# Performance work log

Hardware: AMD Instinct MI355X
Metric: run time of the kernel (lower is better)

## Reference

```python
import jax, jax.numpy as jnp
import numpy as np
import math

B, S, D = 2, 2048, 1024
H, HKV, HD = 16, 4, 64
SF = 4
SD = HD // SF  # sparsity proj dim = 16
TEMP = 1.0
INIT_STD = 0.02


def rope(qk):
    # qk: [b, h, s, d]
    d = qk.shape[-1]
    theta = 1.0 / (10000.0 ** (jnp.arange(0, d, 2, dtype=jnp.float32) / d))  # [d/2]
    s = jnp.arange(qk.shape[2], dtype=jnp.float32)
    freqs = jnp.outer(s, theta)                     # [s, d/2]
    freqs = jnp.concatenate([freqs, freqs], -1)     # [s, d]
    qk1, qk2 = jnp.split(qk, 2, axis=-1)
    rot = jnp.concatenate([-qk2, qk1], -1)
    return qk * jnp.cos(freqs) + rot * jnp.sin(freqs)


def setup_inputs() -> dict:
    key = jax.random.key(0)
    ks = jax.random.split(key, 8)
    x = jax.random.normal(ks[0], (B, S, D), dtype=jnp.float32)
    Wq = jax.random.normal(ks[1], (D, D), dtype=jnp.float32) * INIT_STD
    Wk = jax.random.normal(ks[2], (HKV * HD, D), dtype=jnp.float32) * INIT_STD
    Wv = jax.random.normal(ks[3], (HKV * HD, D), dtype=jnp.float32) * INIT_STD
    Wo = jax.random.normal(ks[4], (D, D), dtype=jnp.float32) * INIT_STD
    bo = jnp.zeros((D,), dtype=jnp.float32)
    Ws = jax.random.normal(ks[5], (SD, HD), dtype=jnp.float32) * INIT_STD
    bs = jnp.zeros((SD,), dtype=jnp.float32)
    return {"x": x, "Wq": Wq, "Wk": Wk, "Wv": Wv, "Wo": Wo, "bo": bo, "Ws": Ws, "bs": bs}


def reference(x, Wq, Wk, Wv, Wo, bo, Ws, bs):
    b, s, _ = x.shape
    # projections (torch Linear: x @ W.T)
    q = (x @ Wq.T).reshape(b, s, H, HD).transpose(0, 2, 1, 3)     # [b,H,s,hd]
    k = (x @ Wk.T).reshape(b, s, HKV, HD).transpose(0, 2, 1, 3)   # [b,Hkv,s,hd]
    v = (x @ Wv.T).reshape(b, s, HKV, HD).transpose(0, 2, 1, 3)
    q = rope(q)
    k = rope(k)
    n_rep = H // HKV
    k = jnp.repeat(k, n_rep, axis=1)  # [b,H,s,hd]
    v = jnp.repeat(v, n_rep, axis=1)
    # low-rank sparsity gate
    q_sp = q @ Ws.T + bs              # [b,H,s,sd]
    k_sp = k @ Ws.T + bs
    sp_scores = jnp.einsum('bhid,bhjd->bhij', q_sp, k_sp) / math.sqrt(SD)
    gate = jax.nn.sigmoid(sp_scores / TEMP)
    attn = jnp.einsum('bhid,bhjd->bhij', q, k) / math.sqrt(HD)
    attn = attn * gate
    causal = jnp.triu(jnp.ones((s, s), dtype=bool), k=1)
    attn = jnp.where(causal, -jnp.inf, attn)
    w = jax.nn.softmax(attn, axis=-1)
    out = jnp.einsum('bhij,bhjd->bhid', w, v)               # [b,H,s,hd]
    out = out.transpose(0, 2, 1, 3).reshape(b, s, H * HD)   # [b,s,D]
    return out @ Wo.T + bo
```

## Files before the change

### kernel.cpp

```cpp
#include <hip/hip_runtime.h>
#include <math.h>

#define B_ 2
#define S_ 2048
#define D_ 1024
#define H_ 16
#define HKV_ 4
#define HD_ 64
#define SD_ 16

typedef __attribute__((ext_vector_type(8))) short bf16x8;
typedef __attribute__((ext_vector_type(4))) float f32x4;
typedef __attribute__((ext_vector_type(8))) unsigned short us8;
typedef __attribute__((ext_vector_type(4))) unsigned short us4;

#define LOG2E 1.4426950408889634f

__device__ __forceinline__ unsigned short f2bf(float f) {
  unsigned int u = __builtin_bit_cast(unsigned int, f);
  u += 0x7fffu + ((u >> 16) & 1u);
  return (unsigned short)(u >> 16);
}

__device__ __forceinline__ void gload16(const unsigned short* g, unsigned short* l) {
  __builtin_amdgcn_global_load_lds(
      (const __attribute__((address_space(1))) unsigned int*)g,
      (__attribute__((address_space(3))) unsigned int*)l, 16, 0, 0);
}

__global__ __launch_bounds__(256) void convert_bf16(
    const float* __restrict__ x, const float* __restrict__ wq,
    const float* __restrict__ wk, const float* __restrict__ wv,
    const float* __restrict__ wo, unsigned short* __restrict__ xb,
    unsigned short* __restrict__ wqkv, unsigned short* __restrict__ wob) {
  const int blk = blockIdx.x;
  const float* src;
  unsigned short* dst;
  int off;
  if (blk < 2048)      { src = x;  dst = xb;             off = blk * 2048; }
  else if (blk < 2560) { src = wq; dst = wqkv;           off = (blk - 2048) * 2048; }
  else if (blk < 2688) { src = wk; dst = wqkv + 1048576; off = (blk - 2560) * 2048; }
  else if (blk < 2816) { src = wv; dst = wqkv + 1310720; off = (blk - 2688) * 2048; }
  else                 { src = wo; dst = wob;            off = (blk - 2816) * 2048; }
  const int i = off + threadIdx.x * 8;
  float4 a = *(const float4*)(src + i);
  float4 b = *(const float4*)(src + i + 4);
  us8 o;
  o[0] = f2bf(a.x); o[1] = f2bf(a.y); o[2] = f2bf(a.z); o[3] = f2bf(a.w);
  o[4] = f2bf(b.x); o[5] = f2bf(b.y); o[6] = f2bf(b.z); o[7] = f2bf(b.w);
  *(us8*)(dst + i) = o;
}

__global__ __launch_bounds__(256) void gemm_bf16(
    const unsigned short* __restrict__ A, const unsigned short* __restrict__ Bm,
    const float* __restrict__ bias, float* __restrict__ C, int N) {
  __shared__ unsigned short As[64 * 64];
  __shared__ unsigned short Bs[128 * 64];
  const int tid = threadIdx.x;
  const int w = tid >> 6, lane = tid & 63;
  const int nm = lane & 15, quad = lane >> 4;
  const int m0 = blockIdx.y * 64, n0 = blockIdx.x * 128;
  const int wn = w * 32;

  f32x4 acc[4][2] = {};
  int arow[2], acol[2], brow[4], bcol[4];
#pragma unroll
  for (int it = 0; it < 2; ++it) {
    int s = it * 256 + tid;
    arow[it] = s >> 3;
    acol[it] = ((s & 7) ^ (arow[it] & 7)) * 8;
  }
#pragma unroll
  for (int it = 0; it < 4; ++it) {
    int s = it * 256 + tid;
    brow[it] = s >> 3;
    bcol[it] = ((s & 7) ^ (brow[it] & 7)) * 8;
  }

  for (int k0 = 0; k0 < 1024; k0 += 64) {
    __syncthreads();
#pragma unroll
    for (int it = 0; it < 2; ++it)
      gload16(A + (size_t)(m0 + arow[it]) * 1024 + k0 + acol[it],
              &As[(it * 256 + w * 64) * 8]);
#pragma unroll
    for (int it = 0; it < 4; ++it)
      gload16(Bm + (size_t)(n0 + brow[it]) * 1024 + k0 + bcol[it],
              &Bs[(it * 256 + w * 64) * 8]);
    __syncthreads();

#pragma unroll
    for (int ks = 0; ks < 2; ++ks) {
      const int cq = ks * 4 + quad;
      bf16x8 af[4], bfr[2];
#pragma unroll
      for (int mi = 0; mi < 4; ++mi) {
        const int m = mi * 16 + nm;
        af[mi] = *(const bf16x8*)&As[(m * 8 + (cq ^ (m & 7))) * 8];
      }
#pragma unroll
      for (int ni = 0; ni < 2; ++ni) {
        const int n = wn + ni * 16 + nm;
        bfr[ni] = *(const bf16x8*)&Bs[(n * 8 + (cq ^ (n & 7))) * 8];
      }
#pragma unroll
      for (int mi = 0; mi < 4; ++mi)
#pragma unroll
        for (int ni = 0; ni < 2; ++ni)
          acc[mi][ni] = __builtin_amdgcn_mfma_f32_16x16x32_bf16(
              af[mi], bfr[ni], acc[mi][ni], 0, 0, 0);
    }
  }

  float bv[2] = {0.f, 0.f};
  if (bias) {
#pragma unroll
    for (int ni = 0; ni < 2; ++ni) bv[ni] = bias[n0 + wn + ni * 16 + nm];
  }
#pragma unroll
  for (int mi = 0; mi < 4; ++mi) {
#pragma unroll
    for (int r = 0; r < 4; ++r) {
      const int row = m0 + mi * 16 + quad * 4 + r;
      float* crow = C + (size_t)row * N + n0 + wn + nm;
#pragma unroll
      for (int ni = 0; ni < 2; ++ni) crow[ni * 16] = acc[mi][ni][r] + bv[ni];
    }
  }
}

__global__ __launch_bounds__(256) void gemm_bf16_128(
    const unsigned short* __restrict__ A, const unsigned short* __restrict__ Bm,
    const float* __restrict__ bias, float* __restrict__ C, int N) {
  __shared__ unsigned short As[128 * 64];
  __shared__ unsigned short Bs[128 * 64];
  const int tid = threadIdx.x;
  const int w = tid >> 6, lane = tid & 63;
  const int nm = lane & 15, quad = lane >> 4;
  const int m0 = blockIdx.y * 128, n0 = blockIdx.x * 128;
  const int wm = (w >> 1) * 64, wn = (w & 1) * 64;

  f32x4 acc[4][4] = {};
  int srow[4], scol[4];
#pragma unroll
  for (int it = 0; it < 4; ++it) {
    int s = it * 256 + tid;
    srow[it] = s >> 3;
    scol[it] = ((s & 7) ^ (srow[it] & 7)) * 8;
  }

  for (int k0 = 0; k0 < 1024; k0 += 64) {
    __syncthreads();
#pragma unroll
    for (int it = 0; it < 4; ++it) {
      gload16(A + (size_t)(m0 + srow[it]) * 1024 + k0 + scol[it],
              &As[(it * 256 + w * 64) * 8]);
      gload16(Bm + (size_t)(n0 + srow[it]) * 1024 + k0 + scol[it],
              &Bs[(it * 256 + w * 64) * 8]);
    }
    __syncthreads();

#pragma unroll
    for (int ks = 0; ks < 2; ++ks) {
      const int cq = ks * 4 + quad;
      bf16x8 af[4], bfr[4];
#pragma unroll
      for (int mi = 0; mi < 4; ++mi) {
        const int m = wm + mi * 16 + nm;
        af[mi] = *(const bf16x8*)&As[(m * 8 + (cq ^ (m & 7))) * 8];
      }
#pragma unroll
      for (int ni = 0; ni < 4; ++ni) {
        const int n = wn + ni * 16 + nm;
        bfr[ni] = *(const bf16x8*)&Bs[(n * 8 + (cq ^ (n & 7))) * 8];
      }
#pragma unroll
      for (int mi = 0; mi < 4; ++mi)
#pragma unroll
        for (int ni = 0; ni < 4; ++ni)
          acc[mi][ni] = __builtin_amdgcn_mfma_f32_16x16x32_bf16(
              af[mi], bfr[ni], acc[mi][ni], 0, 0, 0);
    }
  }

  float bv[4] = {0.f, 0.f, 0.f, 0.f};
  if (bias) {
#pragma unroll
    for (int ni = 0; ni < 4; ++ni) bv[ni] = bias[n0 + wn + ni * 16 + nm];
  }
#pragma unroll
  for (int mi = 0; mi < 4; ++mi) {
#pragma unroll
    for (int r = 0; r < 4; ++r) {
      const int row = m0 + wm + mi * 16 + quad * 4 + r;
      float* crow = C + (size_t)row * N + n0 + wn + nm;
#pragma unroll
      for (int ni = 0; ni < 4; ++ni) crow[ni * 16] = acc[mi][ni][r] + bv[ni];
    }
  }
}

__global__ __launch_bounds__(256) void rope_scatter(
    const float* __restrict__ P, const float* __restrict__ Ws,
    const float* __restrict__ bs, unsigned short* __restrict__ qh,
    unsigned short* __restrict__ kh, unsigned short* __restrict__ qsp,
    unsigned short* __restrict__ ksp) {
  __shared__ float wsl[16 * 64];
  __shared__ float bsl[16];
  __shared__ float rbuf[4][64];
  const int tid = threadIdx.x;
  const int row = blockIdx.x;
  const int b = row >> 11;
  const int s = row & 2047;
  {
    *(float4*)&wsl[tid * 4] = *(const float4*)&Ws[tid * 4];
    if (tid < 16) bsl[tid] = bs[tid];
  }
  __syncthreads();
  const int w = tid >> 6, lane = tid & 63;
  const int i = lane & 31, halfu = lane >> 5;
  const float theta = powf(10000.f, -((float)(2 * i) * (1.f / 64.f)));
  const float f = (float)s * theta;
  const float cf = cosf(f);
  const float sf = sinf(f);
  for (int slot = w; slot < 20; slot += 4) {
    float val = P[(size_t)row * 1536 + slot * 64 + lane];
    float partner = __shfl_xor(val, 32);
    float rot = halfu ? partner : -partner;
    float r = val * cf + rot * sf;
    unsigned short* dst;
    unsigned short* spdst;
    float qscale, spscale;
    if (slot < 16) {
      dst = qh + ((size_t)(b * 16 + slot) * 2048 + s) * 64;
      spdst = qsp + ((size_t)(b * 16 + slot) * 2048 + s) * 16;
      qscale = 0.125f * LOG2E; spscale = 0.25f * LOG2E;
    } else {
      int hh = slot - 16;
      dst = kh + ((size_t)(b * 4 + hh) * 2048 + s) * 64;
      spdst = ksp + ((size_t)(b * 4 + hh) * 2048 + s) * 16;
      qscale = 1.f; spscale = 1.f;
    }
    dst[lane] = f2bf(r * qscale);
    rbuf[w][lane] = r;
    int p = lane >> 4, j = lane & 15;
    float partial = 0.f;
#pragma unroll
    for (int t = 0; t < 16; ++t)
      partial += wsl[j * 64 + p * 16 + t] * rbuf[w][p * 16 + t];
    partial += __shfl_xor(partial, 16);
    partial += __shfl_xor(partial, 32);
    if (p == 0) spdst[j] = f2bf((partial + bsl[j]) * spscale);
  }
}

__global__ __launch_bounds__(256) void v_transpose(
    const float* __restrict__ proj, unsigned short* __restrict__ vt) {
  __shared__ unsigned short t_[64 * 72];
  const int bkv = blockIdx.y;
  const int s0 = blockIdx.x * 64;
  const int b = bkv >> 2, hkv = bkv & 3;
  const int tid = threadIdx.x;
  const int sl = tid >> 2;
  const int c0 = (tid & 3) * 16;
  const float* src = proj + ((size_t)b * 2048 + s0 + sl) * 1536 + 1280 + hkv * 64 + c0;
  us8 o0, o1;
#pragma unroll
  for (int t = 0; t < 8; ++t) { o0[t] = f2bf(src[t]); o1[t] = f2bf(src[8 + t]); }
  *(us8*)&t_[sl * 72 + c0] = o0;
  *(us8*)&t_[sl * 72 + c0 + 8] = o1;
  __syncthreads();
  const int d = tid >> 2;
  const int sc_ = (tid & 3) * 16;
  us8 w0, w1;
#pragma unroll
  for (int t = 0; t < 8; ++t) w0[t] = t_[(sc_ + t) * 72 + d];
#pragma unroll
  for (int t = 0; t < 8; ++t) w1[t] = t_[(sc_ + 8 + t) * 72 + d];
  unsigned short* dst = vt + (size_t)bkv * 131072 + (size_t)d * 2048 + s0 + sc_;
  *(us8*)dst = w0;
  *(us8*)(dst + 8) = w1;
}

template <bool MASK>
__device__ __forceinline__ void attn_tile(
    const unsigned short* __restrict__ Ksb, const unsigned short* __restrict__ Vsb,
    const unsigned short* __restrict__ Kspb_, unsigned short* __restrict__ pw,
    bf16x8 qa0, bf16x8 qa1, bf16x8 qspa, int j0, int qrow0, int nm, int quad,
    int ws, float l_r[4], f32x4 O[4]) {
#pragma unroll
  for (int stl = 0; stl < 2; ++stl) {
    const int st = ws * 2 + stl;
    if (MASK && (j0 + st * 16 > qrow0 + 15)) {
#pragma unroll
      for (int r = 0; r < 4; ++r) {
        const int prow = quad * 4 + r;
        const int chunk = (stl * 2 + (nm >> 3)) ^ ((prow ^ (prow >> 2)) & 3);
        pw[(prow * 4 + chunk) * 8 + (nm & 7)] = 0;
      }
      continue;
    }
    const int krow = st * 16 + nm;
    const int r7 = krow & 7;
    bf16x8 kb0 = *(const bf16x8*)&Ksb[(krow * 8 + (quad ^ r7)) * 8];
    bf16x8 kb1 = *(const bf16x8*)&Ksb[(krow * 8 + ((4 + quad) ^ r7)) * 8];
    bf16x8 gb = *(const bf16x8*)&Kspb_[(krow * 2 + (quad & 1)) * 8];
    f32x4 z = {0.f, 0.f, 0.f, 0.f};
    f32x4 s = __builtin_amdgcn_mfma_f32_16x16x32_bf16(qa0, kb0, z, 0, 0, 0);
    s = __builtin_amdgcn_mfma_f32_16x16x32_bf16(qa1, kb1, s, 0, 0, 0);
    f32x4 g = __builtin_amdgcn_mfma_f32_16x16x32_bf16(qspa, gb, z, 0, 0, 0);
#pragma unroll
    for (int r = 0; r < 4; ++r) {
      float gate = __builtin_amdgcn_rcpf(1.f + __builtin_amdgcn_exp2f(-g[r]));
      float v = s[r] * gate;
      if (MASK) {
        const bool edge = (j0 + st * 16 + 15 > qrow0);
        if (edge) {
          const int col = j0 + st * 16 + nm;
          const int rowg = qrow0 + quad * 4 + r;
          v = (col > rowg) ? -INFINITY : v;
        }
      }
      float p = __builtin_amdgcn_exp2f(v);
      l_r[r] += p;
      const int prow = quad * 4 + r;
      const int chunk = (stl * 2 + (nm >> 3)) ^ ((prow ^ (prow >> 2)) & 3);
      pw[(prow * 4 + chunk) * 8 + (nm & 7)] = f2bf(p);
    }
  }

  bf16x8 pa = *(const bf16x8*)&pw[(nm * 4 + (quad ^ ((nm ^ (nm >> 2)) & 3))) * 8];
#pragma unroll
  for (int dt = 0; dt < 4; ++dt) {
    const int vrow = dt * 16 + nm;
    bf16x8 vb = *(const bf16x8*)&Vsb[(vrow * 8 + ((ws * 4 + quad) ^ (vrow & 7))) * 8];
    O[dt] = __builtin_amdgcn_mfma_f32_16x16x32_bf16(pa, vb, O[dt], 0, 0, 0);
  }
}

__global__ __launch_bounds__(512) void attn_kernel(
    const unsigned short* __restrict__ qh, const unsigned short* __restrict__ kh,
    const unsigned short* __restrict__ vt, const unsigned short* __restrict__ qsp,
    const unsigned short* __restrict__ ksp, unsigned short* __restrict__ ao) {
  __shared__ unsigned short Ks[2][64 * 64];
  __shared__ unsigned short Vs[2][64 * 64];
  __shared__ unsigned short Ksp[2][64 * 16];
  __shared__ unsigned short Pw[8][16 * 32];
  __shared__ float Ox[4][16][64];
  __shared__ float Lx[4][4][64];

  const int tid = threadIdx.x;
  const int w = tid >> 6;
  const int ws = w >> 2;
  const int wr = w & 3;
  const int lane = tid & 63;
  const int nm = lane & 15;
  const int quad = lane >> 4;
  const int bh = blockIdx.y;
  const int b = bh >> 4, h = bh & 15;
  const int hkv = h >> 2;
  const size_t kbase = (size_t)(b * 4 + hkv) * 2048 * 64;
  const size_t vbase = (size_t)(b * 4 + hkv) * 131072;
  const size_t kspb = (size_t)(b * 4 + hkv) * 2048 * 16;

  const int Lc = tid;
  const int sr = Lc >> 3;
  const int sc = ((Lc & 7) ^ (sr & 7)) * 8;
  unsigned short* pw = &Pw[w][0];

#define STAGE(BUF, J0)                                                         \
  {                                                                            \
    gload16(kh + kbase + (size_t)((J0) + sr) * 64 + sc,                        \
            &Ks[BUF][(w * 64) * 8]);                                           \
    gload16(vt + vbase + (size_t)sr * 2048 + (J0) + sc,                        \
            &Vs[BUF][(w * 64) * 8]);                                           \
    if (w < 2) {                                                               \
      gload16(ksp + kspb + (size_t)((J0) + (Lc >> 1)) * 16 + (Lc & 1) * 8,     \
              &Ksp[BUF][w * 512]);                                             \
    }                                                                          \
  }

  const int qxA = 31 - blockIdx.x;
  const int qxB = blockIdx.x;
  const int qrow0A = qxA * 64 + wr * 16;
  const int qrow0B = qxB * 64 + wr * 16;

  const size_t qbA = ((size_t)(b * 16 + h) * 2048 + qrow0A + nm) * 64;
  bf16x8 qa0A = *(const bf16x8*)(qh + qbA + quad * 8);
  bf16x8 qa1A = *(const bf16x8*)(qh + qbA + 32 + quad * 8);
  const size_t qbB = ((size_t)(b * 16 + h) * 2048 + qrow0B + nm) * 64;
  bf16x8 qa0B = *(const bf16x8*)(qh + qbB + quad * 8);
  bf16x8 qa1B = *(const bf16x8*)(qh + qbB + 32 + quad * 8);
  bf16x8 qspaA = {0, 0, 0, 0, 0, 0, 0, 0};
  bf16x8 qspaB = {0, 0, 0, 0, 0, 0, 0, 0};
  if (quad < 2) {
    qspaA = *(const bf16x8*)(qsp + ((size_t)(b * 16 + h) * 2048 + qrow0A + nm) * 16 + quad * 8);
    qspaB = *(const bf16x8*)(qsp + ((size_t)(b * 16 + h) * 2048 + qrow0B + nm) * 16 + quad * 8);
  }

  float l_r[4] = {0.f, 0.f, 0.f, 0.f};
  f32x4 O[4] = {{0.f, 0.f, 0.f, 0.f}, {0.f, 0.f, 0.f, 0.f},
                {0.f, 0.f, 0.f, 0.f}, {0.f, 0.f, 0.f, 0.f}};

  STAGE(0, 0);
  int cur = 0;
  for (int jt = 0; jt < qxA; ++jt) {
    __syncthreads();
    STAGE(cur ^ 1, (jt + 1) * 64)
    attn_tile<false>(&Ks[cur][0], &Vs[cur][0], &Ksp[cur][0], pw,
                     qa0A, qa1A, qspaA, jt * 64, qrow0A, nm, quad, ws, l_r, O);
    cur ^= 1;
  }
  __syncthreads();
  STAGE(cur ^ 1, 0)
  attn_tile<true>(&Ks[cur][0], &Vs[cur][0], &Ksp[cur][0], pw,
                  qa0A, qa1A, qspaA, qxA * 64, qrow0A, nm, quad, ws, l_r, O);
  cur ^= 1;

  if (ws == 1) {
#pragma unroll
    for (int dt = 0; dt < 4; ++dt)
#pragma unroll
      for (int r = 0; r < 4; ++r) Ox[wr][dt * 4 + r][lane] = O[dt][r];
#pragma unroll
    for (int r = 0; r < 4; ++r) Lx[wr][r][lane] = l_r[r];
  }
  __syncthreads();
  if (ws == 0) {
#pragma unroll
    for (int r = 0; r < 4; ++r) {
      float v = l_r[r] + Lx[wr][r][lane];
      v += __shfl_xor(v, 1);
      v += __shfl_xor(v, 2);
      v += __shfl_xor(v, 4);
      v += __shfl_xor(v, 8);
      const float inv = __builtin_amdgcn_rcpf(v);
      const int rowg = qrow0A + quad * 4 + r;
      unsigned short* orow = ao + ((size_t)b * 2048 + rowg) * 1024 + h * 64 + nm;
#pragma unroll
      for (int dt = 0; dt < 4; ++dt)
        orow[dt * 16] = f2bf((O[dt][r] + Ox[wr][dt * 4 + r][lane]) * inv);
    }
  }
#pragma unroll
  for (int dt = 0; dt < 4; ++dt) O[dt] = (f32x4){0.f, 0.f, 0.f, 0.f};
#pragma unroll
  for (int r = 0; r < 4; ++r) l_r[r] = 0.f;

  for (int jt = 0; jt < qxB; ++jt) {
    __syncthreads();
    STAGE(cur ^ 1, (jt + 1) * 64)
    attn_tile<false>(&Ks[cur][0], &Vs[cur][0], &Ksp[cur][0], pw,
                     qa0B, qa1B, qspaB, jt * 64, qrow0B, nm, quad, ws, l_r, O);
    cur ^= 1;
  }
  __syncthreads();
  attn_tile<true>(&Ks[cur][0], &Vs[cur][0], &Ksp[cur][0], pw,
                  qa0B, qa1B, qspaB, qxB * 64, qrow0B, nm, quad, ws, l_r, O);

  if (ws == 1) {
#pragma unroll
    for (int dt = 0; dt < 4; ++dt)
#pragma unroll
      for (int r = 0; r < 4; ++r) Ox[wr][dt * 4 + r][lane] = O[dt][r];
#pragma unroll
    for (int r = 0; r < 4; ++r) Lx[wr][r][lane] = l_r[r];
  }
  __syncthreads();
  if (ws == 0) {
#pragma unroll
    for (int r = 0; r < 4; ++r) {
      float v = l_r[r] + Lx[wr][r][lane];
      v += __shfl_xor(v, 1);
      v += __shfl_xor(v, 2);
      v += __shfl_xor(v, 4);
      v += __shfl_xor(v, 8);
      const float inv = __builtin_amdgcn_rcpf(v);
      const int rowg = qrow0B + quad * 4 + r;
      unsigned short* orow = ao + ((size_t)b * 2048 + rowg) * 1024 + h * 64 + nm;
#pragma unroll
      for (int dt = 0; dt < 4; ++dt)
        orow[dt * 16] = f2bf((O[dt][r] + Ox[wr][dt * 4 + r][lane]) * inv);
    }
  }
#undef STAGE
}

extern "C" void kernel_launch(void* const* d_in, const int* in_sizes, int n_in,
                              void* d_out, int out_size, void* d_ws,
                              size_t ws_size, hipStream_t stream) {
  const float* x = (const float*)d_in[0];
  const float* Wq = (const float*)d_in[1];
  const float* Wk = (const float*)d_in[2];
  const float* Wv = (const float*)d_in[3];
  const float* Wo = (const float*)d_in[4];
  const float* bo = (const float*)d_in[5];
  const float* Ws = (const float*)d_in[6];
  const float* bs = (const float*)d_in[7];
  float* out = (float*)d_out;

  char* wsb = (char*)d_ws;
  float* proj = (float*)wsb;
  unsigned short* aob  = (unsigned short*)wsb;
  unsigned short* qh   = (unsigned short*)(wsb + 25165824);
  unsigned short* kh   = (unsigned short*)(wsb + 33554432);
  unsigned short* vtb  = (unsigned short*)(wsb + 35651584);
  unsigned short* qsp  = (unsigned short*)(wsb + 37748736);
  unsigned short* ksp  = (unsigned short*)(wsb + 39845888);
  unsigned short* xb   = (unsigned short*)(wsb + 40370176);
  unsigned short* wqkv = (unsigned short*)(wsb + 48758784);
  unsigned short* wob  = (unsigned short*)(wsb + 51904512);

  convert_bf16<<<dim3(3328), 256, 0, stream>>>(x, Wq, Wk, Wv, Wo, xb, wqkv, wob);
  gemm_bf16<<<dim3(12, 64), 256, 0, stream>>>(xb, wqkv, nullptr, proj, 1536);
  rope_scatter<<<dim3(4096), 256, 0, stream>>>(proj, Ws, bs, qh, kh, qsp, ksp);
  v_transpose<<<dim3(32, 8), 256, 0, stream>>>(proj, vtb);
  attn_kernel<<<dim3(16, 32), 512, 0, stream>>>(qh, kh, vtb, qsp, ksp, aob);
  gemm_bf16_128<<<dim3(8, 32), 256, 0, stream>>>(aob, wob, bo, out, 1024);
}
```

Baseline: 194.6 us.

## Store QKV projection in bf16, merge rope and V transpose, swap output GEMM tile

The QKV projection GEMM now writes bf16 instead of fp32, which halves the intermediate write and read traffic. Rope and the V transpose are merged into one launch that reads the bf16 projection, so one kernel launch goes away. The output projection switches from the 128x128-tile GEMM to the 64x128-tile GEMM with twice as many blocks. This adds an extra bf16 rounding on q, k and v before rope.

```diff
diff --git a/kernel.cpp b/kernel.cpp
--- a/kernel.cpp
+++ b/kernel.cpp
@@ -20,6 +20,11 @@
   unsigned int u = __builtin_bit_cast(unsigned int, f);
   u += 0x7fffu + ((u >> 16) & 1u);
   return (unsigned short)(u >> 16);
+}
+
+__device__ __forceinline__ float bf2f(unsigned short u) {
+  unsigned int x = ((unsigned int)u) << 16;
+  return __builtin_bit_cast(float, x);
 }
 
 __device__ __forceinline__ void gload16(const unsigned short* g, unsigned short* l) {
@@ -51,6 +56,79 @@
   *(us8*)(dst + i) = o;
 }
 
+__global__ __launch_bounds__(256) void gemm_bf16_p(
+    const unsigned short* __restrict__ A, const unsigned short* __restrict__ Bm,
+    unsigned short* __restrict__ C, int N) {
+  __shared__ unsigned short As[64 * 64];
+  __shared__ unsigned short Bs[128 * 64];
+  const int tid = threadIdx.x;
+  const int w = tid >> 6, lane = tid & 63;
+  const int nm = lane & 15, quad = lane >> 4;
+  const int m0 = blockIdx.y * 64, n0 = blockIdx.x * 128;
+  const int wn = w * 32;
+
+  f32x4 acc[4][2] = {};
+  int arow[2], acol[2], brow[4], bcol[4];
+#pragma unroll
+  for (int it = 0; it < 2; ++it) {
+    int s = it * 256 + tid;
+    arow[it] = s >> 3;
+    acol[it] = ((s & 7) ^ (arow[it] & 7)) * 8;
+  }
+#pragma unroll
+  for (int it = 0; it < 4; ++it) {
+    int s = it * 256 + tid;
+    brow[it] = s >> 3;
+    bcol[it] = ((s & 7) ^ (brow[it] & 7)) * 8;
+  }
+
+  for (int k0 = 0; k0 < 1024; k0 += 64) {
+    __syncthreads();
+#pragma unroll
+    for (int it = 0; it < 2; ++it)
+      gload16(A + (size_t)(m0 + arow[it]) * 1024 + k0 + acol[it],
+              &As[(it * 256 + w * 64) * 8]);
+#pragma unroll
+    for (int it = 0; it < 4; ++it)
+      gload16(Bm + (size_t)(n0 + brow[it]) * 1024 + k0 + bcol[it],
+              &Bs[(it * 256 + w * 64) * 8]);
+    __syncthreads();
+
+#pragma unroll
+    for (int ks = 0; ks < 2; ++ks) {
+      const int cq = ks * 4 + quad;
+      bf16x8 af[4], bfr[2];
+#pragma unroll
+      for (int mi = 0; mi < 4; ++mi) {
+        const int m = mi * 16 + nm;
+        af[mi] = *(const bf16x8*)&As[(m * 8 + (cq ^ (m & 7))) * 8];
+      }
+#pragma unroll
+      for (int ni = 0; ni < 2; ++ni) {
+        const int n = wn + ni * 16 + nm;
+        bfr[ni] = *(const bf16x8*)&Bs[(n * 8 + (cq ^ (n & 7))) * 8];
+      }
+#pragma unroll
+      for (int mi = 0; mi < 4; ++mi)
+#pragma unroll
+        for (int ni = 0; ni < 2; ++ni)
+          acc[mi][ni] = __builtin_amdgcn_mfma_f32_16x16x32_bf16(
+              af[mi], bfr[ni], acc[mi][ni], 0, 0, 0);
+    }
+  }
+
+#pragma unroll
+  for (int mi = 0; mi < 4; ++mi) {
+#pragma unroll
+    for (int r = 0; r < 4; ++r) {
+      const int row = m0 + mi * 16 + quad * 4 + r;
+      unsigned short* crow = C + (size_t)row * N + n0 + wn + nm;
+#pragma unroll
+      for (int ni = 0; ni < 2; ++ni) crow[ni * 16] = f2bf(acc[mi][ni][r]);
+    }
+  }
+}
+
 __global__ __launch_bounds__(256) void gemm_bf16(
     const unsigned short* __restrict__ A, const unsigned short* __restrict__ Bm,
     const float* __restrict__ bias, float* __restrict__ C, int N) {
@@ -129,86 +207,44 @@
   }
 }
 
-__global__ __launch_bounds__(256) void gemm_bf16_128(
-    const unsigned short* __restrict__ A, const unsigned short* __restrict__ Bm,
-    const float* __restrict__ bias, float* __restrict__ C, int N) {
-  __shared__ unsigned short As[128 * 64];
-  __shared__ unsigned short Bs[128 * 64];
-  const int tid = threadIdx.x;
-  const int w = tid >> 6, lane = tid & 63;
-  const int nm = lane & 15, quad = lane >> 4;
-  const int m0 = blockIdx.y * 128, n0 = blockIdx.x * 128;
-  const int wm = (w >> 1) * 64, wn = (w & 1) * 64;
-
-  f32x4 acc[4][4] = {};
-  int srow[4], scol[4];
-#pragma unroll
-  for (int it = 0; it < 4; ++it) {
-    int s = it * 256 + tid;
-    srow[it] = s >> 3;
-    scol[it] = ((s & 7) ^ (srow[it] & 7)) * 8;
-  }
-
-  for (int k0 = 0; k0 < 1024; k0 += 64) {
-    __syncthreads();
-#pragma unroll
-    for (int it = 0; it < 4; ++it) {
-      gload16(A + (size_t)(m0 + srow[it]) * 1024 + k0 + scol[it],
-              &As[(it * 256 + w * 64) * 8]);
-      gload16(Bm + (size_t)(n0 + srow[it]) * 1024 + k0 + scol[it],
-              &Bs[(it * 256 + w * 64) * 8]);
-    }
-    __syncthreads();
-
-#pragma unroll
-    for (int ks = 0; ks < 2; ++ks) {
-      const int cq = ks * 4 + quad;
-      bf16x8 af[4], bfr[4];
-#pragma unroll
-      for (int mi = 0; mi < 4; ++mi) {
-        const int m = wm + mi * 16 + nm;
-        af[mi] = *(const bf16x8*)&As[(m * 8 + (cq ^ (m & 7))) * 8];
-      }
-#pragma unroll
-      for (int ni = 0; ni < 4; ++ni) {
-        const int n = wn + ni * 16 + nm;
-        bfr[ni] = *(const bf16x8*)&Bs[(n * 8 + (cq ^ (n & 7))) * 8];
-      }
-#pragma unroll
-      for (int mi = 0; mi < 4; ++mi)
-#pragma unroll
-        for (int ni = 0; ni < 4; ++ni)
-          acc[mi][ni] = __builtin_amdgcn_mfma_f32_16x16x32_bf16(
-              af[mi], bfr[ni], acc[mi][ni], 0, 0, 0);
-    }
-  }
-
-  float bv[4] = {0.f, 0.f, 0.f, 0.f};
-  if (bias) {
-#pragma unroll
-    for (int ni = 0; ni < 4; ++ni) bv[ni] = bias[n0 + wn + ni * 16 + nm];
-  }
-#pragma unroll
-  for (int mi = 0; mi < 4; ++mi) {
-#pragma unroll
-    for (int r = 0; r < 4; ++r) {
-      const int row = m0 + wm + mi * 16 + quad * 4 + r;
-      float* crow = C + (size_t)row * N + n0 + wn + nm;
-#pragma unroll
-      for (int ni = 0; ni < 4; ++ni) crow[ni * 16] = acc[mi][ni][r] + bv[ni];
-    }
-  }
-}
-
-__global__ __launch_bounds__(256) void rope_scatter(
-    const float* __restrict__ P, const float* __restrict__ Ws,
+__global__ __launch_bounds__(256) void rope_vt(
+    const unsigned short* __restrict__ P, const float* __restrict__ Ws,
     const float* __restrict__ bs, unsigned short* __restrict__ qh,
     unsigned short* __restrict__ kh, unsigned short* __restrict__ qsp,
-    unsigned short* __restrict__ ksp) {
+    unsigned short* __restrict__ ksp, unsigned short* __restrict__ vt) {
   __shared__ float wsl[16 * 64];
   __shared__ float bsl[16];
   __shared__ float rbuf[4][64];
+  __shared__ unsigned short t_[64 * 72];
   const int tid = threadIdx.x;
+
+  if (blockIdx.x >= 4096) {
+    const int t = blockIdx.x - 4096;
+    const int bkv = t >> 5;
+    const int s0 = (t & 31) * 64;
+    const int b = bkv >> 2, hkv = bkv & 3;
+    const int sl = tid >> 2;
+    const int c0 = (tid & 3) * 16;
+    const unsigned short* src =
+        P + ((size_t)b * 2048 + s0 + sl) * 1536 + 1280 + hkv * 64 + c0;
+    us8 o0 = *(const us8*)(src);
+    us8 o1 = *(const us8*)(src + 8);
+    *(us8*)&t_[sl * 72 + c0] = o0;
+    *(us8*)&t_[sl * 72 + c0 + 8] = o1;
+    __syncthreads();
+    const int d = tid >> 2;
+    const int sc_ = (tid & 3) * 16;
+    us8 w0, w1;
+#pragma unroll
+    for (int k = 0; k < 8; ++k) w0[k] = t_[(sc_ + k) * 72 + d];
+#pragma unroll
+    for (int k = 0; k < 8; ++k) w1[k] = t_[(sc_ + 8 + k) * 72 + d];
+    unsigned short* dst = vt + (size_t)bkv * 131072 + (size_t)d * 2048 + s0 + sc_;
+    *(us8*)dst = w0;
+    *(us8*)(dst + 8) = w1;
+    return;
+  }
+
   const int row = blockIdx.x;
   const int b = row >> 11;
   const int s = row & 2047;
@@ -224,7 +260,7 @@
   const float cf = cosf(f);
   const float sf = sinf(f);
   for (int slot = w; slot < 20; slot += 4) {
-    float val = P[(size_t)row * 1536 + slot * 64 + lane];
+    float val = bf2f(P[(size_t)row * 1536 + slot * 64 + lane]);
     float partner = __shfl_xor(val, 32);
     float rot = halfu ? partner : -partner;
     float r = val * cf + rot * sf;
@@ -246,40 +282,12 @@
     int p = lane >> 4, j = lane & 15;
     float partial = 0.f;
 #pragma unroll
-    for (int t = 0; t < 16; ++t)
-      partial += wsl[j * 64 + p * 16 + t] * rbuf[w][p * 16 + t];
+    for (int t2 = 0; t2 < 16; ++t2)
+      partial += wsl[j * 64 + p * 16 + t2] * rbuf[w][p * 16 + t2];
     partial += __shfl_xor(partial, 16);
     partial += __shfl_xor(partial, 32);
     if (p == 0) spdst[j] = f2bf((partial + bsl[j]) * spscale);
   }
-}
-
-__global__ __launch_bounds__(256) void v_transpose(
-    const float* __restrict__ proj, unsigned short* __restrict__ vt) {
-  __shared__ unsigned short t_[64 * 72];
-  const int bkv = blockIdx.y;
-  const int s0 = blockIdx.x * 64;
-  const int b = bkv >> 2, hkv = bkv & 3;
-  const int tid = threadIdx.x;
-  const int sl = tid >> 2;
-  const int c0 = (tid & 3) * 16;
-  const float* src = proj + ((size_t)b * 2048 + s0 + sl) * 1536 + 1280 + hkv * 64 + c0;
-  us8 o0, o1;
-#pragma unroll
-  for (int t = 0; t < 8; ++t) { o0[t] = f2bf(src[t]); o1[t] = f2bf(src[8 + t]); }
-  *(us8*)&t_[sl * 72 + c0] = o0;
-  *(us8*)&t_[sl * 72 + c0 + 8] = o1;
-  __syncthreads();
-  const int d = tid >> 2;
-  const int sc_ = (tid & 3) * 16;
-  us8 w0, w1;
-#pragma unroll
-  for (int t = 0; t < 8; ++t) w0[t] = t_[(sc_ + t) * 72 + d];
-#pragma unroll
-  for (int t = 0; t < 8; ++t) w1[t] = t_[(sc_ + 8 + t) * 72 + d];
-  unsigned short* dst = vt + (size_t)bkv * 131072 + (size_t)d * 2048 + s0 + sc_;
-  *(us8*)dst = w0;
-  *(us8*)(dst + 8) = w1;
 }
 
 template <bool MASK>
@@ -500,7 +508,7 @@
   float* out = (float*)d_out;
 
   char* wsb = (char*)d_ws;
-  float* proj = (float*)wsb;
+  unsigned short* projb = (unsigned short*)wsb;
   unsigned short* aob  = (unsigned short*)wsb;
   unsigned short* qh   = (unsigned short*)(wsb + 25165824);
   unsigned short* kh   = (unsigned short*)(wsb + 33554432);
@@ -512,9 +520,8 @@
   unsigned short* wob  = (unsigned short*)(wsb + 51904512);
 
   convert_bf16<<<dim3(3328), 256, 0, stream>>>(x, Wq, Wk, Wv, Wo, xb, wqkv, wob);
-  gemm_bf16<<<dim3(12, 64), 256, 0, stream>>>(xb, wqkv, nullptr, proj, 1536);
-  rope_scatter<<<dim3(4096), 256, 0, stream>>>(proj, Ws, bs, qh, kh, qsp, ksp);
-  v_transpose<<<dim3(32, 8), 256, 0, stream>>>(proj, vtb);
+  gemm_bf16_p<<<dim3(12, 64), 256, 0, stream>>>(xb, wqkv, projb, 1536);
+  rope_vt<<<dim3(4352), 256, 0, stream>>>(projb, Ws, bs, qh, kh, qsp, ksp, vtb);
   attn_kernel<<<dim3(16, 32), 512, 0, stream>>>(qh, kh, vtb, qsp, ksp, aob);
-  gemm_bf16_128<<<dim3(8, 32), 256, 0, stream>>>(aob, wob, bo, out, 1024);
-}
+  gemm_bf16<<<dim3(8, 64), 256, 0, stream>>>(aob, wob, bo, out, 1024);
+}
```

Result: faster. 184.2 us (-5.4%).
